# Kernel optimization log

Measured on AMD Instinct MI355X. Metric: run time of the kernel, lower is better.

The kernel has to match this reference:

```python
import jax, jax.numpy as jnp
import numpy as np

COST_CLASS = 1.0


def _lsa(cost):
    """linear_sum_assignment clone (Jonker-Volgenant shortest augmenting path),
    matching scipy.optimize.linear_sum_assignment semantics for rectangular inputs."""
    cost = np.asarray(cost, dtype=np.float64)
    transposed = cost.shape[0] > cost.shape[1]
    if transposed:
        cost = cost.T
    nr, nc = cost.shape
    u = np.zeros(nr)
    v = np.zeros(nc)
    path = np.full(nc, -1, dtype=np.int64)
    col4row = np.full(nr, -1, dtype=np.int64)
    row4col = np.full(nc, -1, dtype=np.int64)
    for cur in range(nr):
        i = cur
        SR = np.zeros(nr, dtype=bool)
        SC = np.zeros(nc, dtype=bool)
        d = np.full(nc, np.inf)
        minVal = 0.0
        sink = -1
        while sink == -1:
            SR[i] = True
            rem = ~SC
            r = minVal + cost[i, rem] - u[i] - v[rem]
            dr = d[rem]
            pr = path[rem]
            better = r < dr
            dr[better] = r[better]
            pr[better] = i
            d[rem] = dr
            path[rem] = pr
            remIdx = np.flatnonzero(rem)
            j = remIdx[np.argmin(d[remIdx])]
            minVal = d[j]
            SC[j] = True
            if row4col[j] == -1:
                sink = j
            else:
                i = row4col[j]
        # dual updates (scipy _lsap_body)
        u[cur] += minVal
        mask = SR.copy()
        mask[cur] = False
        u[mask] += minVal - d[col4row[mask]]
        v[SC] -= minVal - d[SC]
        # augment along shortest path
        j = sink
        while True:
            i = path[j]
            row4col[j] = i
            col4row[i], j = j, col4row[i]
            if i == cur:
                break
    if transposed:
        order = np.argsort(col4row)
        return col4row[order], order
    return np.arange(nr), col4row


def setup_inputs() -> dict:
    key = jax.random.key(0)
    k1, k2, k3 = jax.random.split(key, 3)
    bs, Q, T, NC = 32, 256, 128, 2048
    pred_logits = jax.random.normal(k1, (bs, Q, NC), dtype=jnp.float32)
    tgt_labels = jax.random.randint(k2, (bs, T), 0, NC)
    agent_mask = jax.random.randint(k3, (bs, Q), 0, 2).astype(bool)
    return {"pred_logits": pred_logits, "tgt_labels": tgt_labels,
            "agent_mask": agent_mask, "use_background": 0}


def reference(pred_logits, tgt_labels, agent_mask, use_background):
    bs, Q, _ = pred_logits.shape
    T = tgt_labels.shape[1]
    probs = jax.nn.softmax(pred_logits, axis=-1)  # [bs, Q, NC]
    if not use_background:
        probs = jnp.where(agent_mask[:, :, None], probs, 0.0)
    out_prob = probs.reshape(bs * Q, -1)
    tgt_ids = tgt_labels.reshape(-1)                  # concat of all batch labels
    C = COST_CLASS * (-out_prob[:, tgt_ids])          # [bs*Q, bs*T]
    C = C.reshape(bs, Q, bs * T)
    # per-batch Hungarian (same as scipy loop in the original; inherently serial per instance)
    Cn = np.asarray(C)
    rows = np.empty((bs, T), dtype=np.int64)
    cols = np.empty((bs, T), dtype=np.int64)
    for i in range(bs):
        r, c = _lsa(Cn[i, :, i * T:(i + 1) * T])      # [Q, T] block for batch i
        rows[i] = r
        cols[i] = c
    return C, jnp.asarray(rows), jnp.asarray(cols)
```

## Files before the change

kernel.cpp:

```cpp
#include <hip/hip_runtime.h>
#include <hip/hip_bf16.h>
#include <math.h>

#define BS 32
#define QN 256
#define TN 128
#define NCLS 2048
#define NTGT (BS * TN)

__global__ void detect_mask_layout(const unsigned char* __restrict__ m, int* flag) {
    __shared__ int found;
    if (threadIdx.x == 0) found = 0;
    __syncthreads();
    int local = 0;
    for (int i = threadIdx.x; i < BS * QN; i += blockDim.x) {
        if ((i & 3) != 0 && m[i] != 0) local = 1;
    }
    if (local) atomicOr(&found, 1);
    __syncthreads();
    if (threadIdx.x == 0) *flag = found;
}

__global__ __launch_bounds__(256) void compute_C_kernel(
    const float* __restrict__ logits, const int* __restrict__ labels,
    const unsigned char* __restrict__ mask_b, const int* __restrict__ use_bg,
    const int* __restrict__ layout_flag, float* __restrict__ C) {
    __shared__ float prob_sh[NCLS];
    __shared__ int lab_sh[NTGT];
    __shared__ float red[4];

    const int tid = threadIdx.x;
    const int bq = blockIdx.x;
    const float* row = logits + (size_t)bq * NCLS;

    for (int k = tid; k < NTGT; k += 256) lab_sh[k] = labels[k];

    float x[8];
    float m = -INFINITY;
#pragma unroll
    for (int k = 0; k < 8; k++) {
        x[k] = row[tid + k * 256];
        m = fmaxf(m, x[k]);
    }
#pragma unroll
    for (int off = 32; off >= 1; off >>= 1) m = fmaxf(m, __shfl_xor(m, off));
    if ((tid & 63) == 0) red[tid >> 6] = m;
    __syncthreads();
    m = fmaxf(fmaxf(red[0], red[1]), fmaxf(red[2], red[3]));
    __syncthreads();

    float e[8];
    float s = 0.f;
#pragma unroll
    for (int k = 0; k < 8; k++) {
        e[k] = expf(x[k] - m);
        s += e[k];
    }
#pragma unroll
    for (int off = 32; off >= 1; off >>= 1) s += __shfl_xor(s, off);
    if ((tid & 63) == 0) red[tid >> 6] = s;
    __syncthreads();
    s = ((red[0] + red[1]) + red[2]) + red[3];

#pragma unroll
    for (int k = 0; k < 8; k++) prob_sh[tid + k * 256] = e[k] / s;

    const int ub = *use_bg;
    int am;
    if (*layout_flag)
        am = mask_b[bq];
    else
        am = ((const int*)mask_b)[bq];
    const bool zero_row = (ub == 0) && (am == 0);
    __syncthreads();

    float* Crow = C + (size_t)bq * NTGT;
#pragma unroll
    for (int k = 0; k < 16; k++) {
        const int jj = tid + k * 256;
        Crow[jj] = zero_row ? 0.0f : -prob_sh[lab_sh[jj]];
    }
}

__global__ __launch_bounds__(256) void transpose_kernel(const float* __restrict__ C,
                                                        float* __restrict__ CT) {
    __shared__ float tile[TN][65];
    const int b = blockIdx.x;
    const int q0 = blockIdx.y * 64;
    const int tid = threadIdx.x;

    const float* src = C + (size_t)(b * QN + q0) * NTGT + b * TN;
#pragma unroll
    for (int it = 0; it < 32; it++) {
        const int idx = tid + it * 256;
        const int ql = idx >> 7;
        const int i = idx & 127;
        tile[i][ql] = src[(size_t)ql * NTGT + i];
    }
    __syncthreads();
    float* dst = CT + (size_t)b * TN * QN + q0;
#pragma unroll
    for (int it = 0; it < 32; it++) {
        const int idx = tid + it * 256;
        const int i = idx >> 6;
        const int ql = idx & 63;
        dst[(size_t)i * QN + ql] = tile[i][ql];
    }
}

template <int CTRL>
__device__ __forceinline__ double dpp_mov_f64(double x) {
    union { double d; int i[2]; } a, r;
    a.d = x;
    r.i[0] = __builtin_amdgcn_update_dpp(0, a.i[0], CTRL, 0xF, 0xF, true);
    r.i[1] = __builtin_amdgcn_update_dpp(0, a.i[1], CTRL, 0xF, 0xF, true);
    return r.d;
}
__device__ __forceinline__ double read_lane_f64(double x, int srclane) {
    union { double d; int i[2]; } a, r;
    a.d = x;
    r.i[0] = __builtin_amdgcn_readlane(a.i[0], srclane);
    r.i[1] = __builtin_amdgcn_readlane(a.i[1], srclane);
    return r.d;
}

#define QUAD_XOR1 0xB1
#define QUAD_XOR2 0x4E
#define ROW_ROR4  0x124
#define ROW_ROR8  0x128

__global__ __launch_bounds__(64) void lsa_kernel(const float* __restrict__ C,
                                                 const float* __restrict__ CT,
                                                 float* __restrict__ rows_out,
                                                 float* __restrict__ cols_out) {
    const int b = blockIdx.x;
    const int lane = threadIdx.x;
    const int j0 = lane * 4;

    __shared__ float cost_sh[TN * QN];
    __shared__ double u_sh[TN];
    __shared__ int path_sh[QN];
    __shared__ int row4col_sh[QN];
    __shared__ int col4row_sh[TN];

    u_sh[lane] = 0.0;
    u_sh[lane + 64] = 0.0;
    col4row_sh[lane] = -1;
    col4row_sh[lane + 64] = -1;
#pragma unroll
    for (int t = 0; t < 4; t++) row4col_sh[lane + 64 * t] = -1;

    double v0 = 0.0, v1 = 0.0, v2 = 0.0, v3 = 0.0;
    double u0 = 0.0, u1 = 0.0;

    if (CT) {
        const float4* src = (const float4*)(CT + (size_t)b * TN * QN);
        float4* dst = (float4*)cost_sh;
#pragma unroll 8
        for (int it = 0; it < TN * QN / 4 / 64; it++) {
            const int idx = it * 64 + lane;
            dst[idx] = src[idx];
        }
    } else {
        const float* cbsrc = C + (size_t)b * QN * NTGT + b * TN;
        for (int it = 0; it < 512; it++) {
            const int j = it >> 1;
            const int i = lane + 64 * (it & 1);
            cost_sh[i * QN + j] = cbsrc[(size_t)j * NTGT + i];
        }
    }
    __syncthreads();

    for (int cur = 0; cur < TN; cur++) {
        double dv0 = INFINITY, dv1 = INFINITY, dv2 = INFINITY, dv3 = INFINITY;
        double dm0 = INFINITY, dm1 = INFINITY, dm2 = INFINITY, dm3 = INFINITY;
        double du0 = 0.0, du1 = 0.0;
        int sc = 0, sr = 0;
        int p0 = 0, p1 = 0, p2 = 0, p3 = 0;
        const int4 rcv = *(const int4*)&row4col_sh[j0];
        if (lane == (cur >> 1)) sr = 1 << (cur & 1);

        int i = cur;
        double m_d = 0.0;
        bool need_reduce = true;
        unsigned long long B0 = 0, B1 = 0, B2 = 0, B3 = 0;
        int sink;

        while (true) {
            const float4 cc = *(const float4*)(cost_sh + i * QN + j0);
            const double ui = u_sh[i];

            const double ca0 = ((m_d + (double)cc.x) - ui) - v0;
            const double ca1 = ((m_d + (double)cc.y) - ui) - v1;
            const double ca2 = ((m_d + (double)cc.z) - ui) - v2;
            const double ca3 = ((m_d + (double)cc.w) - ui) - v3;
            const bool i0 = !(sc & 1) && (ca0 < dv0);
            const bool i1 = !(sc & 2) && (ca1 < dv1);
            const bool i2 = !(sc & 4) && (ca2 < dv2);
            const bool i3 = !(sc & 8) && (ca3 < dv3);
            const unsigned long long anyI =
                __ballot(i0) | __ballot(i1) | __ballot(i2) | __ballot(i3);
            if (i0) { dv0 = ca0; dm0 = ca0; p0 = i; }
            if (i1) { dv1 = ca1; dm1 = ca1; p1 = i; }
            if (i2) { dv2 = ca2; dm2 = ca2; p2 = i; }
            if (i3) { dv3 = ca3; dm3 = ca3; p3 = i; }

            if (anyI != 0ull || need_reduce) {
                double lm = fmin(fmin(dm0, dm1), fmin(dm2, dm3));
                lm = fmin(lm, dpp_mov_f64<QUAD_XOR1>(lm));
                lm = fmin(lm, dpp_mov_f64<QUAD_XOR2>(lm));
                lm = fmin(lm, dpp_mov_f64<ROW_ROR4>(lm));
                lm = fmin(lm, dpp_mov_f64<ROW_ROR8>(lm));
                const double r0 = read_lane_f64(lm, 0);
                const double r1 = read_lane_f64(lm, 16);
                const double r2 = read_lane_f64(lm, 32);
                const double r3 = read_lane_f64(lm, 48);
                m_d = fmin(fmin(r0, r1), fmin(r2, r3));
                B0 = __ballot(dm0 == m_d);
                B1 = __ballot(dm1 == m_d);
                B2 = __ballot(dm2 == m_d);
                B3 = __ballot(dm3 == m_d);
            }

            int jmin = 0x7fffffff;
            if (B0) { const int c = ((__ffsll((long long)B0) - 1) << 2) + 0; jmin = c < jmin ? c : jmin; }
            if (B1) { const int c = ((__ffsll((long long)B1) - 1) << 2) + 1; jmin = c < jmin ? c : jmin; }
            if (B2) { const int c = ((__ffsll((long long)B2) - 1) << 2) + 2; jmin = c < jmin ? c : jmin; }
            if (B3) { const int c = ((__ffsll((long long)B3) - 1) << 2) + 3; jmin = c < jmin ? c : jmin; }
            const int owner = jmin >> 2;
            const int slot = jmin & 3;
            const unsigned long long bit = 1ull << owner;
            if (slot == 0) B0 &= ~bit;
            else if (slot == 1) B1 &= ~bit;
            else if (slot == 2) B2 &= ~bit;
            else B3 &= ~bit;

            if (lane == owner) {
                sc |= 1 << slot;
                if (slot == 0) dm0 = INFINITY;
                else if (slot == 1) dm1 = INFINITY;
                else if (slot == 2) dm2 = INFINITY;
                else dm3 = INFINITY;
            }

            const int sa = (slot & 1) ? rcv.y : rcv.x;
            const int sb = (slot & 1) ? rcv.w : rcv.z;
            const int rcsel = (slot & 2) ? sb : sa;
            const int krc = __builtin_amdgcn_readlane(rcsel, owner);
            if (krc < 0) { sink = jmin; break; }

            if (lane == (krc >> 1)) {
                if (krc & 1) { du1 = m_d; sr |= 2; }
                else { du0 = m_d; sr |= 1; }
            }
            i = krc;
            need_reduce = ((B0 | B1 | B2 | B3) == 0ull);
        }

        path_sh[lane] = p0;
        path_sh[lane + 64] = p1;
        path_sh[lane + 128] = p2;
        path_sh[lane + 192] = p3;
        if (sc & 1) v0 -= m_d - dv0;
        if (sc & 2) v1 -= m_d - dv1;
        if (sc & 4) v2 -= m_d - dv2;
        if (sc & 8) v3 -= m_d - dv3;
        if (sr & 1) u0 += (2 * lane == cur) ? m_d : (m_d - du0);
        if (sr & 2) u1 += (2 * lane + 1 == cur) ? m_d : (m_d - du1);
        u_sh[2 * lane] = u0;
        u_sh[2 * lane + 1] = u1;
        __syncthreads();

        if (lane == 0) {
            int j = sink;
            while (true) {
                const int pi = path_sh[(j & 3) * 64 + (j >> 2)];
                row4col_sh[j] = pi;
                const int nj = col4row_sh[pi];
                col4row_sh[pi] = j;
                j = nj;
                if (pi == cur) break;
            }
        }
        __syncthreads();
    }

#pragma unroll
    for (int t = 0; t < 2; t++) {
        const int ii = lane + 64 * t;
        const int myv = col4row_sh[ii];
        int rank = 0;
        for (int t2 = 0; t2 < TN; t2++) rank += (col4row_sh[t2] < myv) ? 1 : 0;
        rows_out[b * TN + rank] = (float)myv;
        cols_out[b * TN + rank] = (float)ii;
    }
}

extern "C" void kernel_launch(void* const* d_in, const int* in_sizes, int n_in,
                              void* d_out, int out_size, void* d_ws, size_t ws_size,
                              hipStream_t stream) {
    const float* logits = (const float*)d_in[0];
    const int* labels = (const int*)d_in[1];
    const unsigned char* mask_b = (const unsigned char*)d_in[2];
    const int* use_bg = (const int*)d_in[3];

    float* C = (float*)d_out;
    float* rows_out = C + (size_t)BS * QN * NTGT;
    float* cols_out = rows_out + BS * TN;

    int* flag = (int*)d_ws;
    const size_t ct_off = 4096;
    const size_t ct_bytes = (size_t)BS * TN * QN * sizeof(float);
    const bool useCT = ws_size >= ct_off + ct_bytes;
    float* CT = useCT ? (float*)((char*)d_ws + ct_off) : nullptr;

    detect_mask_layout<<<1, 256, 0, stream>>>(mask_b, flag);
    compute_C_kernel<<<BS * QN, 256, 0, stream>>>(logits, labels, mask_b, use_bg, flag, C);
    if (useCT) {
        dim3 tg(BS, QN / 64);
        transpose_kernel<<<tg, 256, 0, stream>>>(C, CT);
    }
    lsa_kernel<<<BS, 64, 0, stream>>>(C, CT, rows_out, cols_out);
}
```

Measured before the change: 1.145 ms.

## Keep LSA duals and assignments in registers, prefetch next cost rows

Moves u, row4col, col4row and path out of shared memory into per-lane registers, read with readlane broadcasts. The augmentation walk now runs wave-wide instead of on lane 0 between two barriers, so both per-row __syncthreads calls go away. It also speculatively prefetches the cost rows for the next two candidate columns into double-buffered registers, to hide LDS latency on the serial Dijkstra chain. The cost is extra register pressure and more scalar work per iteration.

```diff
diff --git a/kernel.cpp b/kernel.cpp
--- a/kernel.cpp
+++ b/kernel.cpp
@@ -123,11 +123,36 @@
     r.i[1] = __builtin_amdgcn_readlane(a.i[1], srclane);
     return r.d;
 }
+__device__ __forceinline__ int sel4(const int4& r, int slot) {
+    const int a = (slot & 1) ? r.y : r.x;
+    const int b = (slot & 1) ? r.w : r.z;
+    return (slot & 2) ? b : a;
+}
+__device__ __forceinline__ int pick_first(unsigned long long B0, unsigned long long B1,
+                                          unsigned long long B2, unsigned long long B3) {
+    int jmin = 0x7fffffff;
+    if (B0) { const int c = ((__ffsll((long long)B0) - 1) << 2) + 0; jmin = c < jmin ? c : jmin; }
+    if (B1) { const int c = ((__ffsll((long long)B1) - 1) << 2) + 1; jmin = c < jmin ? c : jmin; }
+    if (B2) { const int c = ((__ffsll((long long)B2) - 1) << 2) + 2; jmin = c < jmin ? c : jmin; }
+    if (B3) { const int c = ((__ffsll((long long)B3) - 1) << 2) + 3; jmin = c < jmin ? c : jmin; }
+    return jmin;
+}
 
 #define QUAD_XOR1 0xB1
 #define QUAD_XOR2 0x4E
 #define ROW_ROR4  0x124
 #define ROW_ROR8  0x128
+
+#define ENSURE_SLOT(JS, CS, JN)                                                       \
+    do {                                                                              \
+        if ((JN) != 0x7fffffff && (JS) != (JN)) {                                     \
+            const int _k = __builtin_amdgcn_readlane(sel4(rc, (JN) & 3), (JN) >> 2);  \
+            if (_k >= 0) {                                                            \
+                CS = *(const float4*)(cost_sh + _k * QN + j0);                        \
+                JS = (JN);                                                            \
+            }                                                                         \
+        }                                                                             \
+    } while (0)
 
 __global__ __launch_bounds__(64) void lsa_kernel(const float* __restrict__ C,
                                                  const float* __restrict__ CT,
@@ -138,20 +163,12 @@
     const int j0 = lane * 4;
 
     __shared__ float cost_sh[TN * QN];
-    __shared__ double u_sh[TN];
-    __shared__ int path_sh[QN];
-    __shared__ int row4col_sh[QN];
     __shared__ int col4row_sh[TN];
-
-    u_sh[lane] = 0.0;
-    u_sh[lane + 64] = 0.0;
-    col4row_sh[lane] = -1;
-    col4row_sh[lane + 64] = -1;
-#pragma unroll
-    for (int t = 0; t < 4; t++) row4col_sh[lane + 64 * t] = -1;
 
     double v0 = 0.0, v1 = 0.0, v2 = 0.0, v3 = 0.0;
     double u0 = 0.0, u1 = 0.0;
+    int4 rc = make_int4(-1, -1, -1, -1);
+    int c0 = -1, c1 = -1;
 
     if (CT) {
         const float4* src = (const float4*)(CT + (size_t)b * TN * QN);
@@ -171,13 +188,14 @@
     }
     __syncthreads();
 
+    float4 first_cc = *(const float4*)(cost_sh + j0);
+
     for (int cur = 0; cur < TN; cur++) {
         double dv0 = INFINITY, dv1 = INFINITY, dv2 = INFINITY, dv3 = INFINITY;
         double dm0 = INFINITY, dm1 = INFINITY, dm2 = INFINITY, dm3 = INFINITY;
         double du0 = 0.0, du1 = 0.0;
         int sc = 0, sr = 0;
         int p0 = 0, p1 = 0, p2 = 0, p3 = 0;
-        const int4 rcv = *(const int4*)&row4col_sh[j0];
         if (lane == (cur >> 1)) sr = 1 << (cur & 1);
 
         int i = cur;
@@ -186,10 +204,13 @@
         unsigned long long B0 = 0, B1 = 0, B2 = 0, B3 = 0;
         int sink;
 
+        float4 cc = first_cc;
+        double ui = read_lane_f64((cur & 1) ? u1 : u0, cur >> 1);
+
+        int jsA = -1, jsB = -1, ph = 0;
+        float4 csA, csB;
+
         while (true) {
-            const float4 cc = *(const float4*)(cost_sh + i * QN + j0);
-            const double ui = u_sh[i];
-
             const double ca0 = ((m_d + (double)cc.x) - ui) - v0;
             const double ca1 = ((m_d + (double)cc.y) - ui) - v1;
             const double ca2 = ((m_d + (double)cc.z) - ui) - v2;
@@ -198,8 +219,7 @@
             const bool i1 = !(sc & 2) && (ca1 < dv1);
             const bool i2 = !(sc & 4) && (ca2 < dv2);
             const bool i3 = !(sc & 8) && (ca3 < dv3);
-            const unsigned long long anyI =
-                __ballot(i0) | __ballot(i1) | __ballot(i2) | __ballot(i3);
+            const unsigned long long anyI = __ballot(i0 | i1 | i2 | i3);
             if (i0) { dv0 = ca0; dm0 = ca0; p0 = i; }
             if (i1) { dv1 = ca1; dm1 = ca1; p1 = i; }
             if (i2) { dv2 = ca2; dm2 = ca2; p2 = i; }
@@ -222,11 +242,7 @@
                 B3 = __ballot(dm3 == m_d);
             }
 
-            int jmin = 0x7fffffff;
-            if (B0) { const int c = ((__ffsll((long long)B0) - 1) << 2) + 0; jmin = c < jmin ? c : jmin; }
-            if (B1) { const int c = ((__ffsll((long long)B1) - 1) << 2) + 1; jmin = c < jmin ? c : jmin; }
-            if (B2) { const int c = ((__ffsll((long long)B2) - 1) << 2) + 2; jmin = c < jmin ? c : jmin; }
-            if (B3) { const int c = ((__ffsll((long long)B3) - 1) << 2) + 3; jmin = c < jmin ? c : jmin; }
+            const int jmin = pick_first(B0, B1, B2, B3);
             const int owner = jmin >> 2;
             const int slot = jmin & 3;
             const unsigned long long bit = 1ull << owner;
@@ -243,11 +259,13 @@
                 else dm3 = INFINITY;
             }
 
-            const int sa = (slot & 1) ? rcv.y : rcv.x;
-            const int sb = (slot & 1) ? rcv.w : rcv.z;
-            const int rcsel = (slot & 2) ? sb : sa;
-            const int krc = __builtin_amdgcn_readlane(rcsel, owner);
+            const int krc = __builtin_amdgcn_readlane(sel4(rc, slot), owner);
             if (krc < 0) { sink = jmin; break; }
+
+            if (jmin == jsA) cc = csA;
+            else if (jmin == jsB) cc = csB;
+            else cc = *(const float4*)(cost_sh + krc * QN + j0);
+            ui = read_lane_f64((krc & 1) ? u1 : u0, krc >> 1);
 
             if (lane == (krc >> 1)) {
                 if (krc & 1) { du1 = m_d; sr |= 2; }
@@ -255,35 +273,66 @@
             }
             i = krc;
             need_reduce = ((B0 | B1 | B2 | B3) == 0ull);
+
+            {
+                const int jn1 = pick_first(B0, B1, B2, B3);
+                int jn2 = 0x7fffffff;
+                if (jn1 != 0x7fffffff) {
+                    unsigned long long T0 = B0, T1 = B1, T2 = B2, T3 = B3;
+                    const unsigned long long nb = 1ull << (jn1 >> 2);
+                    const int nsl = jn1 & 3;
+                    if (nsl == 0) T0 &= ~nb;
+                    else if (nsl == 1) T1 &= ~nb;
+                    else if (nsl == 2) T2 &= ~nb;
+                    else T3 &= ~nb;
+                    jn2 = pick_first(T0, T1, T2, T3);
+                }
+                if (ph == 0) {
+                    ENSURE_SLOT(jsB, csB, jn1);
+                    ENSURE_SLOT(jsA, csA, jn2);
+                } else {
+                    ENSURE_SLOT(jsA, csA, jn1);
+                    ENSURE_SLOT(jsB, csB, jn2);
+                }
+                ph ^= 1;
+            }
         }
 
-        path_sh[lane] = p0;
-        path_sh[lane + 64] = p1;
-        path_sh[lane + 128] = p2;
-        path_sh[lane + 192] = p3;
         if (sc & 1) v0 -= m_d - dv0;
         if (sc & 2) v1 -= m_d - dv1;
         if (sc & 4) v2 -= m_d - dv2;
         if (sc & 8) v3 -= m_d - dv3;
         if (sr & 1) u0 += (2 * lane == cur) ? m_d : (m_d - du0);
         if (sr & 2) u1 += (2 * lane + 1 == cur) ? m_d : (m_d - du1);
-        u_sh[2 * lane] = u0;
-        u_sh[2 * lane + 1] = u1;
-        __syncthreads();
-
-        if (lane == 0) {
-            int j = sink;
-            while (true) {
-                const int pi = path_sh[(j & 3) * 64 + (j >> 2)];
-                row4col_sh[j] = pi;
-                const int nj = col4row_sh[pi];
-                col4row_sh[pi] = j;
-                j = nj;
-                if (pi == cur) break;
-            }
+
+        if (cur + 1 < TN) first_cc = *(const float4*)(cost_sh + (cur + 1) * QN + j0);
+
+        int j = sink;
+        while (true) {
+            const int sl = j & 3;
+            const int ow = j >> 2;
+            const int pa = (sl & 1) ? p1 : p0;
+            const int pb = (sl & 1) ? p3 : p2;
+            const int pi = __builtin_amdgcn_readlane((sl & 2) ? pb : pa, ow);
+            if (lane == ow) {
+                if (sl == 0) rc.x = pi;
+                else if (sl == 1) rc.y = pi;
+                else if (sl == 2) rc.z = pi;
+                else rc.w = pi;
+            }
+            const int nj = __builtin_amdgcn_readlane((pi & 1) ? c1 : c0, pi >> 1);
+            if (lane == (pi >> 1)) {
+                if (pi & 1) c1 = j;
+                else c0 = j;
+            }
+            j = nj;
+            if (pi == cur) break;
         }
-        __syncthreads();
-    }
+    }
+
+    col4row_sh[2 * lane] = c0;
+    col4row_sh[2 * lane + 1] = c1;
+    __syncthreads();
 
 #pragma unroll
     for (int t = 0; t < 2; t++) {
```

After: 1.452 ms. 26.8% more time.

## Fuse transposed cost write into softmax kernel and vectorize loads/stores

Applied to the files above, without the earlier changes.

Removes the separate transpose kernel by having each compute_C block write its own batch-diagonal column slice into CT directly. It also vectorizes the logits loads and C stores with float4, and drops the shared-memory label staging in favour of direct int4 label reads. This saves a kernel launch and a re-read of the diagonal blocks of C. The price is strided scattered stores into CT with a stride of QN floats. The LSA kernel likely dominates the runtime, so the gain is limited to the preprocessing stage.

```diff
diff --git a/kernel.cpp b/kernel.cpp
--- a/kernel.cpp
+++ b/kernel.cpp
@@ -24,24 +24,20 @@
 __global__ __launch_bounds__(256) void compute_C_kernel(
     const float* __restrict__ logits, const int* __restrict__ labels,
     const unsigned char* __restrict__ mask_b, const int* __restrict__ use_bg,
-    const int* __restrict__ layout_flag, float* __restrict__ C) {
+    const int* __restrict__ layout_flag, float* __restrict__ C,
+    float* __restrict__ CT) {
     __shared__ float prob_sh[NCLS];
-    __shared__ int lab_sh[NTGT];
     __shared__ float red[4];
 
     const int tid = threadIdx.x;
     const int bq = blockIdx.x;
     const float* row = logits + (size_t)bq * NCLS;
 
-    for (int k = tid; k < NTGT; k += 256) lab_sh[k] = labels[k];
-
-    float x[8];
-    float m = -INFINITY;
-#pragma unroll
-    for (int k = 0; k < 8; k++) {
-        x[k] = row[tid + k * 256];
-        m = fmaxf(m, x[k]);
-    }
+    const float4 xa = ((const float4*)row)[tid];
+    const float4 xb = ((const float4*)row)[tid + 256];
+
+    float m = fmaxf(fmaxf(fmaxf(xa.x, xa.y), fmaxf(xa.z, xa.w)),
+                    fmaxf(fmaxf(xb.x, xb.y), fmaxf(xb.z, xb.w)));
 #pragma unroll
     for (int off = 32; off >= 1; off >>= 1) m = fmaxf(m, __shfl_xor(m, off));
     if ((tid & 63) == 0) red[tid >> 6] = m;
@@ -49,21 +45,24 @@
     m = fmaxf(fmaxf(red[0], red[1]), fmaxf(red[2], red[3]));
     __syncthreads();
 
-    float e[8];
-    float s = 0.f;
-#pragma unroll
-    for (int k = 0; k < 8; k++) {
-        e[k] = expf(x[k] - m);
-        s += e[k];
-    }
+    float4 ea, eb;
+    ea.x = expf(xa.x - m);
+    ea.y = expf(xa.y - m);
+    ea.z = expf(xa.z - m);
+    ea.w = expf(xa.w - m);
+    eb.x = expf(xb.x - m);
+    eb.y = expf(xb.y - m);
+    eb.z = expf(xb.z - m);
+    eb.w = expf(xb.w - m);
+    float s = ((ea.x + ea.y) + (ea.z + ea.w)) + ((eb.x + eb.y) + (eb.z + eb.w));
 #pragma unroll
     for (int off = 32; off >= 1; off >>= 1) s += __shfl_xor(s, off);
     if ((tid & 63) == 0) red[tid >> 6] = s;
     __syncthreads();
     s = ((red[0] + red[1]) + red[2]) + red[3];
 
-#pragma unroll
-    for (int k = 0; k < 8; k++) prob_sh[tid + k * 256] = e[k] / s;
+    ((float4*)prob_sh)[tid] = make_float4(ea.x / s, ea.y / s, ea.z / s, ea.w / s);
+    ((float4*)prob_sh)[tid + 256] = make_float4(eb.x / s, eb.y / s, eb.z / s, eb.w / s);
 
     const int ub = *use_bg;
     int am;
@@ -75,36 +74,30 @@
     __syncthreads();
 
     float* Crow = C + (size_t)bq * NTGT;
-#pragma unroll
-    for (int k = 0; k < 16; k++) {
-        const int jj = tid + k * 256;
-        Crow[jj] = zero_row ? 0.0f : -prob_sh[lab_sh[jj]];
-    }
-}
-
-__global__ __launch_bounds__(256) void transpose_kernel(const float* __restrict__ C,
-                                                        float* __restrict__ CT) {
-    __shared__ float tile[TN][65];
-    const int b = blockIdx.x;
-    const int q0 = blockIdx.y * 64;
-    const int tid = threadIdx.x;
-
-    const float* src = C + (size_t)(b * QN + q0) * NTGT + b * TN;
-#pragma unroll
-    for (int it = 0; it < 32; it++) {
-        const int idx = tid + it * 256;
-        const int ql = idx >> 7;
-        const int i = idx & 127;
-        tile[i][ql] = src[(size_t)ql * NTGT + i];
-    }
-    __syncthreads();
-    float* dst = CT + (size_t)b * TN * QN + q0;
-#pragma unroll
-    for (int it = 0; it < 32; it++) {
-        const int idx = tid + it * 256;
-        const int i = idx >> 6;
-        const int ql = idx & 63;
-        dst[(size_t)i * QN + ql] = tile[i][ql];
+    const int4* lab4 = (const int4*)labels;
+    if (zero_row) {
+        const float4 z = make_float4(0.f, 0.f, 0.f, 0.f);
+#pragma unroll
+        for (int k = 0; k < 4; k++) ((float4*)Crow)[tid + k * 256] = z;
+    } else {
+#pragma unroll
+        for (int k = 0; k < 4; k++) {
+            const int4 l = lab4[tid + k * 256];
+            float4 o;
+            o.x = -prob_sh[l.x];
+            o.y = -prob_sh[l.y];
+            o.z = -prob_sh[l.z];
+            o.w = -prob_sh[l.w];
+            ((float4*)Crow)[tid + k * 256] = o;
+        }
+    }
+
+    if (CT != nullptr && tid < TN) {
+        const int bb = bq >> 8;
+        const int q = bq & 255;
+        const int lab = labels[bb * TN + tid];
+        CT[(size_t)bb * TN * QN + (size_t)tid * QN + q] =
+            zero_row ? 0.0f : -prob_sh[lab];
     }
 }
 
@@ -315,10 +308,6 @@
     float* CT = useCT ? (float*)((char*)d_ws + ct_off) : nullptr;
 
     detect_mask_layout<<<1, 256, 0, stream>>>(mask_b, flag);
-    compute_C_kernel<<<BS * QN, 256, 0, stream>>>(logits, labels, mask_b, use_bg, flag, C);
-    if (useCT) {
-        dim3 tg(BS, QN / 64);
-        transpose_kernel<<<tg, 256, 0, stream>>>(C, CT);
-    }
+    compute_C_kernel<<<BS * QN, 256, 0, stream>>>(logits, labels, mask_b, use_bg, flag, C, CT);
     lsa_kernel<<<BS, 64, 0, stream>>>(C, CT, rows_out, cols_out);
 }
```

Result: no change. 1.151 ms (+0.5%).
